# Optimization experiments

Hardware: AMD Instinct MI355X
Metric: run time of the kernel (lower is better)

The kernel has to match this reference:

```python
import jax, jax.numpy as jnp
import numpy as np

N = 50000          # nodes
E = 800000         # edges (before self-loops)
IN_DIM = 128
HIDDEN = 128
HEADS = 8
C = HIDDEN // HEADS  # 16, per-head dim
NEG_SLOPE = 0.2


def setup_inputs() -> dict:
    key = jax.random.key(0)
    ks = jax.random.split(key, 12)
    s = 0.1
    return {
        "x": jax.random.normal(ks[0], (N, IN_DIM), jnp.float32),
        "W1": jax.random.normal(ks[1], (IN_DIM, HIDDEN), jnp.float32) * s,
        "b1": jnp.zeros((HIDDEN,), jnp.float32),
        "att_l1": jax.random.normal(ks[2], (1, HEADS, C), jnp.float32) * s,
        "att_r1": jax.random.normal(ks[3], (1, HEADS, C), jnp.float32) * s,
        "W2": jax.random.normal(ks[4], (HIDDEN, HIDDEN), jnp.float32) * s,
        "b2": jnp.zeros((HIDDEN,), jnp.float32),
        "att_l2": jax.random.normal(ks[5], (1, HEADS, C), jnp.float32) * s,
        "att_r2": jax.random.normal(ks[6], (1, HEADS, C), jnp.float32) * s,
        "fcW": jax.random.normal(ks[7], (HIDDEN, 1), jnp.float32) * s,
        "fcb": jnp.zeros((1,), jnp.float32),
        "edge_index": jax.random.randint(ks[8], (2, E), 0, N, jnp.int32),
    }


def supergat_layer(h, W, b, att_l, att_r, src, dst):
    """SuperGATConv (attention_type='MX', concat=True), eval mode (no dropout).
    src/dst already include self-loops. h: [N, F_in]."""
    xt = (h @ W).reshape(N, HEADS, C)            # [N, H, C]
    x_j = xt[src]                                # source (message) feats [Etot, H, C]
    x_i = xt[dst]                                # target feats           [Etot, H, C]
    # MX attention: alpha = (a_l . x_j + a_r . x_i) * sigmoid(x_i . x_j)
    logits = jnp.sum(x_i * x_j, axis=-1)         # [Etot, H]
    alpha = jnp.sum(x_j * att_l, axis=-1) + jnp.sum(x_i * att_r, axis=-1)
    alpha = alpha * jax.nn.sigmoid(logits)
    alpha = jax.nn.leaky_relu(alpha, NEG_SLOPE)
    # segment softmax over incoming edges of each target node
    amax = jax.lax.stop_gradient(jax.ops.segment_max(alpha, dst, num_segments=N))
    ex = jnp.exp(alpha - amax[dst])
    denom = jax.ops.segment_sum(ex, dst, num_segments=N)
    attn = ex / (denom[dst] + 1e-16)             # [Etot, H]
    out = jax.ops.segment_sum(x_j * attn[..., None], dst, num_segments=N)  # [N, H, C]
    return out.reshape(N, HEADS * C) + b


def reference(x, W1, b1, att_l1, att_r1, W2, b2, att_l2, att_r2, fcW, fcb, edge_index):
    # add self-loops once (SuperGATConv add_self_loops=True)
    loops = jnp.arange(N, dtype=edge_index.dtype)
    src = jnp.concatenate([edge_index[0], loops])
    dst = jnp.concatenate([edge_index[1], loops])
    gelu = lambda t: jax.nn.gelu(t, approximate=False)
    h = gelu(supergat_layer(x, W1, b1, att_l1, att_r1, src, dst))   # dropout = identity (eval)
    h = gelu(supergat_layer(h, W2, b2, att_l2, att_r2, src, dst))
    return h @ fcW + fcb                          # [N, 1]
```

## Files before the change

### kernel.cpp

```cpp
#include <hip/hip_runtime.h>
#include <hip/hip_fp16.h>
#include <math.h>

#define N_NODES 50000
#define N_EDGES 800000
#define ETOT (N_EDGES + N_NODES)
#define F 128
#define SCAN_B 256
#define NSCAN ((N_NODES + SCAN_B - 1) / SCAN_B)
#define LOG2E 1.44269504088896341f

typedef _Float16 h2 __attribute__((ext_vector_type(2)));
typedef _Float16 h8 __attribute__((ext_vector_type(8)));
typedef float f4v __attribute__((ext_vector_type(4)));

__device__ __forceinline__ float dpp_xor1(float v) {
    int b = __builtin_amdgcn_update_dpp(0, __float_as_int(v), 0xB1, 0xF, 0xF, true);
    return v + __int_as_float(b);
}


__global__ void k_prep(const float* __restrict__ x, const float* __restrict__ W1,
                       const float* __restrict__ W2, _Float16* __restrict__ x16,
                       _Float16* __restrict__ WT1, _Float16* __restrict__ WT2,
                       int* __restrict__ counts) {
    int tid = blockIdx.x * 256 + threadIdx.x;
    if (tid < 16384) {
        int k = tid >> 7, c = tid & 127;
        WT1[c * 128 + k] = (_Float16)W1[tid];
    } else if (tid < 32768) {
        int j = tid - 16384;
        int k = j >> 7, c = j & 127;
        WT2[c * 128 + k] = (_Float16)W2[j];
    } else if (tid < 832768) {
        int i = tid - 32768;
        const float4* xp = (const float4*)x + (size_t)i * 2;
        float4 a = xp[0], b = xp[1];
        _Float16 hh[8] = {(_Float16)a.x, (_Float16)a.y, (_Float16)a.z, (_Float16)a.w,
                          (_Float16)b.x, (_Float16)b.y, (_Float16)b.z, (_Float16)b.w};
        *(uint4*)(x16 + (size_t)i * 8) = *(const uint4*)hh;
    } else if (tid < 832768 + N_NODES) {
        counts[tid - 832768] = 0;
    }
}


__global__ void k_count(const int* __restrict__ ei, int* __restrict__ counts) {
    int base = (blockIdx.x * 256 + threadIdx.x) * 8;
    if (base < N_EDGES) {
        int4 a = *(const int4*)(ei + N_EDGES + base);
        int4 b = *(const int4*)(ei + N_EDGES + base + 4);
        atomicAdd(&counts[a.x], 1); atomicAdd(&counts[a.y], 1);
        atomicAdd(&counts[a.z], 1); atomicAdd(&counts[a.w], 1);
        atomicAdd(&counts[b.x], 1); atomicAdd(&counts[b.y], 1);
        atomicAdd(&counts[b.z], 1); atomicAdd(&counts[b.w], 1);
    }
}

__global__ void k_scan1(const int* __restrict__ counts, int* __restrict__ indptr,
                        int* __restrict__ bsums) {
    __shared__ int s[SCAN_B];
    int i = blockIdx.x * SCAN_B + threadIdx.x;
    int v = (i < N_NODES) ? (counts[i] + 1) : 0;
    s[threadIdx.x] = v;
    __syncthreads();
    #pragma unroll
    for (int off = 1; off < SCAN_B; off <<= 1) {
        int t = (threadIdx.x >= off) ? s[threadIdx.x - off] : 0;
        __syncthreads();
        s[threadIdx.x] += t;
        __syncthreads();
    }
    if (i < N_NODES) indptr[i] = s[threadIdx.x] - v;
    if (threadIdx.x == SCAN_B - 1) bsums[blockIdx.x] = s[SCAN_B - 1];
}

__global__ void k_scan2(int* __restrict__ bsums) {
    __shared__ int s[SCAN_B];
    int v = (threadIdx.x < NSCAN) ? bsums[threadIdx.x] : 0;
    s[threadIdx.x] = v;
    __syncthreads();
    #pragma unroll
    for (int off = 1; off < SCAN_B; off <<= 1) {
        int t = (threadIdx.x >= off) ? s[threadIdx.x - off] : 0;
        __syncthreads();
        s[threadIdx.x] += t;
        __syncthreads();
    }
    if (threadIdx.x < NSCAN) bsums[threadIdx.x] = s[threadIdx.x] - v;
}

__global__ void k_scan3_fill(int* __restrict__ indptr, const int* __restrict__ bsums,
                             int* __restrict__ fill, int* __restrict__ srcs) {
    int i = blockIdx.x * SCAN_B + threadIdx.x;
    if (i < N_NODES) {
        int p = indptr[i] + bsums[blockIdx.x];
        indptr[i] = p;
        fill[i] = p + 1;
        srcs[p] = i;
    }
    if (i == 0) indptr[N_NODES] = ETOT;
}

__global__ void k_fill_edges(const int* __restrict__ ei, int* __restrict__ fill,
                             int* __restrict__ srcs) {
    int base = (blockIdx.x * 256 + threadIdx.x) * 8;
    if (base < N_EDGES) {
        int4 sa = *(const int4*)(ei + base);
        int4 sb = *(const int4*)(ei + base + 4);
        int4 da = *(const int4*)(ei + N_EDGES + base);
        int4 db = *(const int4*)(ei + N_EDGES + base + 4);
        int p0 = atomicAdd(&fill[da.x], 1);
        int p1 = atomicAdd(&fill[da.y], 1);
        int p2 = atomicAdd(&fill[da.z], 1);
        int p3 = atomicAdd(&fill[da.w], 1);
        int p4 = atomicAdd(&fill[db.x], 1);
        int p5 = atomicAdd(&fill[db.y], 1);
        int p6 = atomicAdd(&fill[db.z], 1);
        int p7 = atomicAdd(&fill[db.w], 1);
        srcs[p0] = sa.x; srcs[p1] = sa.y; srcs[p2] = sa.z; srcs[p3] = sa.w;
        srcs[p4] = sb.x; srcs[p5] = sb.y; srcs[p6] = sb.z; srcs[p7] = sb.w;
    }
}


__global__ __launch_bounds__(256) void k_gemm(const _Float16* __restrict__ Ah,
                                              const _Float16* __restrict__ WT,
                                              _Float16* __restrict__ Ch) {
    __shared__ _Float16 Wl[128][132];
    int t = threadIdx.x;

    const uint4* WT4 = (const uint4*)WT;
    #pragma unroll
    for (int jj = 0; jj < 8; ++jj) {
        int i = t + jj * 256;
        int c = i >> 4;
        int k8 = i & 15;
        *(uint4*)&Wl[c][k8 * 8] = WT4[i];
    }
    __syncthreads();

    int wid = t >> 6, lane = t & 63;
    int rbase = blockIdx.x * 64 + wid * 16;
    int rA = rbase + (lane & 15);
    if (rA >= N_NODES) rA = N_NODES - 1;
    int koff = (lane >> 4) * 8;

    const _Float16* Ar = Ah + (size_t)rA * 128;
    h8 af[4];
    #pragma unroll
    for (int kc = 0; kc < 4; ++kc)
        af[kc] = *(const h8*)(Ar + kc * 32 + koff);

    f4v acc[8];
    #pragma unroll
    for (int ct = 0; ct < 8; ++ct) acc[ct] = f4v{0.f, 0.f, 0.f, 0.f};

    int colb = lane & 15;
    #pragma unroll
    for (int ct = 0; ct < 8; ++ct) {
        const _Float16* wrow = &Wl[ct * 16 + colb][koff];
        #pragma unroll
        for (int kc = 0; kc < 4; ++kc) {
            h8 bf = *(const h8*)(wrow + kc * 32);
            acc[ct] = __builtin_amdgcn_mfma_f32_16x16x32_f16(af[kc], bf, acc[ct], 0, 0, 0);
        }
    }

    int rout = rbase + (lane >> 4) * 4;
    #pragma unroll
    for (int r = 0; r < 4; ++r) {
        int row = rout + r;
        if (row < N_NODES) {
            _Float16* Crow = Ch + (size_t)row * 128;
            #pragma unroll
            for (int ct = 0; ct < 8; ++ct)
                Crow[ct * 16 + colb] = (_Float16)acc[ct][r];
        }
    }
}


__global__ __launch_bounds__(256) void k_attn(
    const unsigned char* __restrict__ xt16,
    const int* __restrict__ indptr, const int* __restrict__ srcs,
    const float* __restrict__ att_l, const float* __restrict__ att_r,
    const float* __restrict__ bias, float* __restrict__ out,
    _Float16* __restrict__ outh,
    const float* __restrict__ fcW, const float* __restrict__ fcb, int mode) {

    int wid = threadIdx.x >> 6;
    int lane = threadIdx.x & 63;
    int node = blockIdx.x * 4 + wid;
    if (node >= N_NODES) return;
    int sub = lane >> 4;
    int sl  = lane & 15;

    uint4 xa = *(const uint4*)(xt16 + (size_t)node * 256 + sl * 16);
    h2 xi_h2[4];
    xi_h2[0] = __builtin_bit_cast(h2, xa.x); xi_h2[1] = __builtin_bit_cast(h2, xa.y);
    xi_h2[2] = __builtin_bit_cast(h2, xa.z); xi_h2[3] = __builtin_bit_cast(h2, xa.w);

    const float4* arp = (const float4*)(att_r + sl * 8);
    const float4* alp = (const float4*)(att_l + sl * 8);
    float4 r0 = arp[0], r1 = arp[1];
    float4 l0 = alp[0], l1 = alp[1];
    float rs = (float)xi_h2[0].x*r0.x + (float)xi_h2[0].y*r0.y
             + (float)xi_h2[1].x*r0.z + (float)xi_h2[1].y*r0.w
             + (float)xi_h2[2].x*r1.x + (float)xi_h2[2].y*r1.y
             + (float)xi_h2[3].x*r1.z + (float)xi_h2[3].y*r1.w;
    float ri = LOG2E * dpp_xor1(rs);
    h2 al_h2[4];
    al_h2[0] = h2{(_Float16)(l0.x*LOG2E), (_Float16)(l0.y*LOG2E)};
    al_h2[1] = h2{(_Float16)(l0.z*LOG2E), (_Float16)(l0.w*LOG2E)};
    al_h2[2] = h2{(_Float16)(l1.x*LOG2E), (_Float16)(l1.y*LOG2E)};
    al_h2[3] = h2{(_Float16)(l1.z*LOG2E), (_Float16)(l1.w*LOG2E)};

    float d = 0.f;
    float o[8];
    #pragma unroll
    for (int k = 0; k < 8; ++k) o[k] = 0.f;

    int beg = indptr[node], end = indptr[node + 1];
    int nstep = (end - beg + 3) >> 2;

    int idx = beg + sub;
    bool v0 = idx < end;
    int j0 = srcs[v0 ? idx : beg];
    uint4 ra0 = *(const uint4*)(xt16 + (size_t)j0 * 256 + sl * 16);
    int idx1 = idx + 4;
    bool v1 = idx1 < end;
    int j1 = srcs[v1 ? idx1 : beg];

    for (int s = 0; s < nstep; ++s) {
        uint4 ra1 = *(const uint4*)(xt16 + (size_t)j1 * 256 + sl * 16);
        int idx2 = idx1 + 4;
        bool v2 = idx2 < end;
        int j2 = srcs[v2 ? idx2 : beg];

        h2 xj[4];
        xj[0] = __builtin_bit_cast(h2, ra0.x); xj[1] = __builtin_bit_cast(h2, ra0.y);
        xj[2] = __builtin_bit_cast(h2, ra0.z); xj[3] = __builtin_bit_cast(h2, ra0.w);

        float lg = 0.f, lj = 0.f;
        #pragma unroll
        for (int k = 0; k < 4; ++k) {
            lg = __builtin_amdgcn_fdot2(xi_h2[k], xj[k], lg, false);
            lj = __builtin_amdgcn_fdot2(al_h2[k], xj[k], lj, false);
        }
        lg = dpp_xor1(lg);
        lj = dpp_xor1(lj);

        float sg = __builtin_amdgcn_rcpf(1.f + __builtin_amdgcn_exp2f(-lg * LOG2E));
        float a = (lj + ri) * sg;
        a = fmaxf(a, 0.f) + 0.2f * fminf(a, 0.f);
        a = v0 ? a : -1e30f;
        float e = __builtin_amdgcn_exp2f(a);
        d += e;
        #pragma unroll
        for (int k = 0; k < 4; ++k) {
            o[2*k]   += e * (float)xj[k].x;
            o[2*k+1] += e * (float)xj[k].y;
        }

        ra0 = ra1; v0 = v1; v1 = v2; j1 = j2; idx1 = idx2;
    }

    d += __shfl_xor(d, 16);
    d += __shfl_xor(d, 32);
    #pragma unroll
    for (int k = 0; k < 8; ++k) {
        o[k] += __shfl_xor(o[k], 16);
        o[k] += __shfl_xor(o[k], 32);
    }

    float inv = __builtin_amdgcn_rcpf(d + 1e-16f);
    const float4* bbp = (const float4*)(bias + sl * 8);
    float4 b0 = bbp[0], b1 = bbp[1];
    float bb[8] = {b0.x, b0.y, b0.z, b0.w, b1.x, b1.y, b1.z, b1.w};
    float g[8];
    #pragma unroll
    for (int k = 0; k < 8; ++k) {
        float v = o[k] * inv + bb[k];
        g[k] = 0.5f * v * (1.f + erff(v * 0.70710678118654752f));
    }

    if (mode == 0) {
        if (sub == 0) {
            _Float16 hh[8];
            #pragma unroll
            for (int k = 0; k < 8; ++k) hh[k] = (_Float16)g[k];
            *(uint4*)(outh + (size_t)node * 128 + sl * 8) = *(const uint4*)hh;
        }
    } else {
        const float4* fwp = (const float4*)(fcW + sl * 8);
        float4 f0 = fwp[0], f1 = fwp[1];
        float p = g[0]*f0.x + g[1]*f0.y + g[2]*f0.z + g[3]*f0.w
                + g[4]*f1.x + g[5]*f1.y + g[6]*f1.z + g[7]*f1.w;
        p += __shfl_xor(p, 1);
        p += __shfl_xor(p, 2);
        p += __shfl_xor(p, 4);
        p += __shfl_xor(p, 8);
        if (lane == 0) out[node] = p + fcb[0];
    }
}


extern "C" void kernel_launch(void* const* d_in, const int* in_sizes, int n_in,
                              void* d_out, int out_size, void* d_ws, size_t ws_size,
                              hipStream_t stream) {
    const float* x     = (const float*)d_in[0];
    const float* W1    = (const float*)d_in[1];
    const float* b1    = (const float*)d_in[2];
    const float* attl1 = (const float*)d_in[3];
    const float* attr1 = (const float*)d_in[4];
    const float* W2    = (const float*)d_in[5];
    const float* b2    = (const float*)d_in[6];
    const float* attl2 = (const float*)d_in[7];
    const float* attr2 = (const float*)d_in[8];
    const float* fcW   = (const float*)d_in[9];
    const float* fcb   = (const float*)d_in[10];
    const int*   ei    = (const int*)d_in[11];
    float* outp = (float*)d_out;

    _Float16* x16  = (_Float16*)d_ws;
    _Float16* h16  = x16 + (size_t)N_NODES * F;
    _Float16* xt16 = h16 + (size_t)N_NODES * F;
    _Float16* WT1  = xt16 + (size_t)N_NODES * F;
    _Float16* WT2  = WT1 + F * F;
    int* indptr = (int*)(WT2 + F * F);
    int* fill   = indptr + (N_NODES + 1);
    int* srcs   = fill + N_NODES;
    int* bsums  = srcs + ETOT;
    int* counts = fill;

    int nb_e8 = (N_EDGES / 8 + 255) / 256;
    int nb_p  = (832768 + N_NODES + 255) / 256;

    k_prep<<<nb_p, 256, 0, stream>>>(x, W1, W2, x16, WT1, WT2, counts);
    k_count<<<nb_e8, 256, 0, stream>>>(ei, counts);
    k_scan1<<<NSCAN, SCAN_B, 0, stream>>>(counts, indptr, bsums);
    k_scan2<<<1, SCAN_B, 0, stream>>>(bsums);
    k_scan3_fill<<<NSCAN, SCAN_B, 0, stream>>>(indptr, bsums, fill, srcs);
    k_fill_edges<<<nb_e8, 256, 0, stream>>>(ei, fill, srcs);

    int nb_g = (N_NODES + 63) / 64;
    int nb_a = (N_NODES + 3) / 4;

    k_gemm<<<nb_g, 256, 0, stream>>>(x16, WT1, xt16);
    k_attn<<<nb_a, 256, 0, stream>>>((const unsigned char*)xt16, indptr, srcs,
                                     attl1, attr1, b1, outp, h16, fcW, fcb, 0);
    k_gemm<<<nb_g, 256, 0, stream>>>(h16, WT2, xt16);
    k_attn<<<nb_a, 256, 0, stream>>>((const unsigned char*)xt16, indptr, srcs,
                                     attl2, attr2, b2, outp, h16, fcW, fcb, 1);
}
```

Before: 297.3 us.

## Record per-edge slot during counting and scatter CSR without second atomic pass

The counting kernel now stores the atomicAdd return value as each edge's position within its destination segment, so the fill kernel becomes a plain scatter using indptr plus that position instead of a second round of contended atomics. The attention epilogue is also split so each of the four sub-lanes computes GELU for two channels rather than every lane computing all eight, and the outputs are written as half2 with an extra shuffle reduction stage. The cost is an extra per-edge position array that is written and then read back, plus an indirect indptr lookup per edge.

```diff
diff --git a/kernel.cpp b/kernel.cpp
--- a/kernel.cpp
+++ b/kernel.cpp
@@ -23,7 +23,7 @@
 __global__ void k_prep(const float* __restrict__ x, const float* __restrict__ W1,
                        const float* __restrict__ W2, _Float16* __restrict__ x16,
                        _Float16* __restrict__ WT1, _Float16* __restrict__ WT2,
-                       int* __restrict__ counts) {
+                       int* __restrict__ fill0) {
     int tid = blockIdx.x * 256 + threadIdx.x;
     if (tid < 16384) {
         int k = tid >> 7, c = tid & 127;
@@ -40,20 +40,21 @@
                           (_Float16)b.x, (_Float16)b.y, (_Float16)b.z, (_Float16)b.w};
         *(uint4*)(x16 + (size_t)i * 8) = *(const uint4*)hh;
     } else if (tid < 832768 + N_NODES) {
-        counts[tid - 832768] = 0;
-    }
-}
-
-
-__global__ void k_count(const int* __restrict__ ei, int* __restrict__ counts) {
-    int base = (blockIdx.x * 256 + threadIdx.x) * 8;
+        fill0[tid - 832768] = 0;
+    }
+}
+
+
+__global__ void k_pos(const int* __restrict__ ei, int* __restrict__ fill0,
+                      int* __restrict__ pos) {
+    int base = (blockIdx.x * 256 + threadIdx.x) * 4;
     if (base < N_EDGES) {
-        int4 a = *(const int4*)(ei + N_EDGES + base);
-        int4 b = *(const int4*)(ei + N_EDGES + base + 4);
-        atomicAdd(&counts[a.x], 1); atomicAdd(&counts[a.y], 1);
-        atomicAdd(&counts[a.z], 1); atomicAdd(&counts[a.w], 1);
-        atomicAdd(&counts[b.x], 1); atomicAdd(&counts[b.y], 1);
-        atomicAdd(&counts[b.z], 1); atomicAdd(&counts[b.w], 1);
+        int4 d4 = *(const int4*)(ei + N_EDGES + base);
+        int p0 = atomicAdd(&fill0[d4.x], 1);
+        int p1 = atomicAdd(&fill0[d4.y], 1);
+        int p2 = atomicAdd(&fill0[d4.z], 1);
+        int p3 = atomicAdd(&fill0[d4.w], 1);
+        *(int4*)(pos + base) = make_int4(p0, p1, p2, p3);
     }
 }
 
@@ -91,35 +92,34 @@
 }
 
 __global__ void k_scan3_fill(int* __restrict__ indptr, const int* __restrict__ bsums,
-                             int* __restrict__ fill, int* __restrict__ srcs) {
+                             int* __restrict__ srcs) {
     int i = blockIdx.x * SCAN_B + threadIdx.x;
     if (i < N_NODES) {
         int p = indptr[i] + bsums[blockIdx.x];
         indptr[i] = p;
-        fill[i] = p + 1;
         srcs[p] = i;
     }
     if (i == 0) indptr[N_NODES] = ETOT;
 }
 
-__global__ void k_fill_edges(const int* __restrict__ ei, int* __restrict__ fill,
-                             int* __restrict__ srcs) {
+__global__ void k_scatter(const int* __restrict__ ei, const int* __restrict__ indptr,
+                          const int* __restrict__ pos, int* __restrict__ srcs) {
     int base = (blockIdx.x * 256 + threadIdx.x) * 8;
     if (base < N_EDGES) {
         int4 sa = *(const int4*)(ei + base);
         int4 sb = *(const int4*)(ei + base + 4);
         int4 da = *(const int4*)(ei + N_EDGES + base);
         int4 db = *(const int4*)(ei + N_EDGES + base + 4);
-        int p0 = atomicAdd(&fill[da.x], 1);
-        int p1 = atomicAdd(&fill[da.y], 1);
-        int p2 = atomicAdd(&fill[da.z], 1);
-        int p3 = atomicAdd(&fill[da.w], 1);
-        int p4 = atomicAdd(&fill[db.x], 1);
-        int p5 = atomicAdd(&fill[db.y], 1);
-        int p6 = atomicAdd(&fill[db.z], 1);
-        int p7 = atomicAdd(&fill[db.w], 1);
-        srcs[p0] = sa.x; srcs[p1] = sa.y; srcs[p2] = sa.z; srcs[p3] = sa.w;
-        srcs[p4] = sb.x; srcs[p5] = sb.y; srcs[p6] = sb.z; srcs[p7] = sb.w;
+        int4 pa = *(const int4*)(pos + base);
+        int4 pb = *(const int4*)(pos + base + 4);
+        srcs[indptr[da.x] + 1 + pa.x] = sa.x;
+        srcs[indptr[da.y] + 1 + pa.y] = sa.y;
+        srcs[indptr[da.z] + 1 + pa.z] = sa.z;
+        srcs[indptr[da.w] + 1 + pa.w] = sa.w;
+        srcs[indptr[db.x] + 1 + pb.x] = sb.x;
+        srcs[indptr[db.y] + 1 + pb.y] = sb.y;
+        srcs[indptr[db.z] + 1 + pb.z] = sb.z;
+        srcs[indptr[db.w] + 1 + pb.w] = sb.w;
     }
 }
 
@@ -275,32 +275,29 @@
     }
 
     float inv = __builtin_amdgcn_rcpf(d + 1e-16f);
-    const float4* bbp = (const float4*)(bias + sl * 8);
-    float4 b0 = bbp[0], b1 = bbp[1];
-    float bb[8] = {b0.x, b0.y, b0.z, b0.w, b1.x, b1.y, b1.z, b1.w};
-    float g[8];
-    #pragma unroll
-    for (int k = 0; k < 8; ++k) {
-        float v = o[k] * inv + bb[k];
-        g[k] = 0.5f * v * (1.f + erff(v * 0.70710678118654752f));
-    }
+    float oa, ob;
+    if (sub == 0)      { oa = o[0]; ob = o[1]; }
+    else if (sub == 1) { oa = o[2]; ob = o[3]; }
+    else if (sub == 2) { oa = o[4]; ob = o[5]; }
+    else               { oa = o[6]; ob = o[7]; }
+    float2 bb2 = ((const float2*)bias)[sl * 4 + sub];
+    float va = oa * inv + bb2.x;
+    float vb = ob * inv + bb2.y;
+    float ga = 0.5f * va * (1.f + erff(va * 0.70710678118654752f));
+    float gb = 0.5f * vb * (1.f + erff(vb * 0.70710678118654752f));
 
     if (mode == 0) {
-        if (sub == 0) {
-            _Float16 hh[8];
-            #pragma unroll
-            for (int k = 0; k < 8; ++k) hh[k] = (_Float16)g[k];
-            *(uint4*)(outh + (size_t)node * 128 + sl * 8) = *(const uint4*)hh;
-        }
+        h2 hh = h2{(_Float16)ga, (_Float16)gb};
+        *(h2*)(outh + (size_t)node * 128 + sl * 8 + sub * 2) = hh;
     } else {
-        const float4* fwp = (const float4*)(fcW + sl * 8);
-        float4 f0 = fwp[0], f1 = fwp[1];
-        float p = g[0]*f0.x + g[1]*f0.y + g[2]*f0.z + g[3]*f0.w
-                + g[4]*f1.x + g[5]*f1.y + g[6]*f1.z + g[7]*f1.w;
+        float2 fw2 = ((const float2*)fcW)[sl * 4 + sub];
+        float p = ga * fw2.x + gb * fw2.y;
         p += __shfl_xor(p, 1);
         p += __shfl_xor(p, 2);
         p += __shfl_xor(p, 4);
         p += __shfl_xor(p, 8);
+        p += __shfl_xor(p, 16);
+        p += __shfl_xor(p, 32);
         if (lane == 0) out[node] = p + fcb[0];
     }
 }
@@ -329,20 +326,21 @@
     _Float16* WT1  = xt16 + (size_t)N_NODES * F;
     _Float16* WT2  = WT1 + F * F;
     int* indptr = (int*)(WT2 + F * F);
-    int* fill   = indptr + (N_NODES + 1);
-    int* srcs   = fill + N_NODES;
+    int* fill0  = indptr + (N_NODES + 1);
+    int* srcs   = fill0 + N_NODES;
     int* bsums  = srcs + ETOT;
-    int* counts = fill;
-
+    int* pos    = bsums + NSCAN;
+
+    int nb_e4 = (N_EDGES / 4 + 255) / 256;
     int nb_e8 = (N_EDGES / 8 + 255) / 256;
     int nb_p  = (832768 + N_NODES + 255) / 256;
 
-    k_prep<<<nb_p, 256, 0, stream>>>(x, W1, W2, x16, WT1, WT2, counts);
-    k_count<<<nb_e8, 256, 0, stream>>>(ei, counts);
-    k_scan1<<<NSCAN, SCAN_B, 0, stream>>>(counts, indptr, bsums);
+    k_prep<<<nb_p, 256, 0, stream>>>(x, W1, W2, x16, WT1, WT2, fill0);
+    k_pos<<<nb_e4, 256, 0, stream>>>(ei, fill0, pos);
+    k_scan1<<<NSCAN, SCAN_B, 0, stream>>>(fill0, indptr, bsums);
     k_scan2<<<1, SCAN_B, 0, stream>>>(bsums);
-    k_scan3_fill<<<NSCAN, SCAN_B, 0, stream>>>(indptr, bsums, fill, srcs);
-    k_fill_edges<<<nb_e8, 256, 0, stream>>>(ei, fill, srcs);
+    k_scan3_fill<<<NSCAN, SCAN_B, 0, stream>>>(indptr, bsums, srcs);
+    k_scatter<<<nb_e8, 256, 0, stream>>>(ei, indptr, pos, srcs);
 
     int nb_g = (N_NODES + 63) / 64;
     int nb_a = (N_NODES + 3) / 4;
```

After: 264.7 us. 1.12x faster.
